# Kernel tuning notes

Hardware: AMD Instinct MI355X
Metric: run time of the kernel (lower is better)

The kernel has to match this reference:

```python
import jax, jax.numpy as jnp
import numpy as np

D_MODEL = 1472
N_HEADS = 6
D_KV = 64
INNER = N_HEADS * D_KV
NUM_BUCKETS = 32
MAX_DIST = 128


def _relative_position_bucket(relative_position, bidirectional=True,
                              num_buckets=NUM_BUCKETS, max_distance=MAX_DIST):
    ret = jnp.zeros_like(relative_position)
    if bidirectional:
        num_buckets //= 2
        ret = ret + (relative_position > 0).astype(jnp.int32) * num_buckets
        rel = jnp.abs(relative_position)
    else:
        rel = -jnp.minimum(relative_position, 0)
    max_exact = num_buckets // 2
    is_small = rel < max_exact
    rel_f = jnp.maximum(rel, 1).astype(jnp.float32)
    large = max_exact + (
        jnp.log(rel_f / max_exact) / np.log(max_distance / max_exact)
        * (num_buckets - max_exact)
    ).astype(jnp.int32)
    large = jnp.minimum(large, num_buckets - 1)
    return ret + jnp.where(is_small, rel, large)


def _position_bias(q_len, k_len, rel_bias):
    # rel_bias: [num_buckets, n_heads]
    ctx = jnp.arange(q_len)[:, None]
    mem = jnp.arange(k_len)[None, :]
    buckets = _relative_position_bucket(mem - ctx, bidirectional=True)
    values = rel_bias[buckets]                 # [Q, K, H]
    return jnp.transpose(values, (2, 0, 1))[None]  # [1, H, Q, K]


def setup_inputs() -> dict:
    key = jax.random.key(0)
    ks = jax.random.split(key, 8)
    B, S = 4, 2048
    scale = 0.02
    return {
        "kv_sequences": jax.random.normal(ks[0], (B, S, D_MODEL), jnp.float32),
        "q_sequences": jax.random.normal(ks[1], (B, S, D_MODEL), jnp.float32),
        "mask": jnp.zeros((B, 1, S, S), jnp.float32),
        "WQ": jax.random.normal(ks[2], (D_MODEL, INNER), jnp.float32) * scale,
        "WK": jax.random.normal(ks[3], (D_MODEL, INNER), jnp.float32) * scale,
        "WV": jax.random.normal(ks[4], (D_MODEL, INNER), jnp.float32) * scale,
        "WO": jax.random.normal(ks[5], (INNER, D_MODEL), jnp.float32) * scale,
        "rel_bias": jax.random.normal(ks[6], (NUM_BUCKETS, N_HEADS), jnp.float32) * scale,
    }


def reference(kv_sequences, q_sequences, mask, WQ, WK, WV, WO, rel_bias):
    B, Kl, _ = kv_sequences.shape
    Ql = q_sequences.shape[1]
    # projections -> [B, H, L, d_kv]
    q = (q_sequences @ WQ).reshape(B, Ql, N_HEADS, D_KV).transpose(0, 2, 1, 3)
    k = (kv_sequences @ WK).reshape(B, Kl, N_HEADS, D_KV).transpose(0, 2, 1, 3)
    v = (kv_sequences @ WV).reshape(B, Kl, N_HEADS, D_KV).transpose(0, 2, 1, 3)
    # T5-style: no 1/sqrt(d) scaling
    logits = jnp.einsum("bhqd,bhkd->bhqk", q, k)
    logits = logits + _position_bias(Ql, Kl, rel_bias)
    logits = logits + mask
    attn = jax.nn.softmax(logits.astype(jnp.float32), axis=-1).astype(logits.dtype)
    out = jnp.einsum("bhqk,bhkd->bhqd", attn, v)
    out = out.transpose(0, 2, 1, 3).reshape(B, Ql, INNER)
    return out @ WO
```

## Files before the change

kernel.cpp:

```cpp
#include <hip/hip_runtime.h>
#include <hip/hip_fp16.h>
#include <cstdint>

#define DM    1472
#define NH    6
#define DKV   64
#define INNER 384
#define BATCH 4
#define SEQ   2048
#define LOG2E 1.4426950408889634f

typedef __attribute__((ext_vector_type(8))) _Float16 half8;
typedef __attribute__((ext_vector_type(4))) _Float16 half4;
typedef __attribute__((ext_vector_type(4))) float f32x4;

__device__ __forceinline__ int swz64(int row, int b)  { return b ^ (((row >> 1) & 3) << 4); }
__device__ __forceinline__ int swz128(int row, int b) { return b ^ ((row & 7) << 4); }

__device__ __forceinline__ void gload16(const void* g, const void* l) {
  __builtin_amdgcn_global_load_lds((const __attribute__((address_space(1))) void*)g,
                                   (__attribute__((address_space(3))) void*)l, 16, 0, 0);
}

__global__ void prep_weights(const float* __restrict__ WQ, const float* __restrict__ WK,
                             const float* __restrict__ WV, const float* __restrict__ WO,
                             _Float16* __restrict__ WqT, _Float16* __restrict__ WkT,
                             _Float16* __restrict__ WvT, _Float16* __restrict__ WoT) {
  int idx = blockIdx.x * blockDim.x + threadIdx.x;
  const int per = DM * INNER;
  if (idx >= 4 * per) return;
  int which = idx / per;
  int i = idx - which * per;
  if (which < 3) {
    const float* W = which == 0 ? WQ : (which == 1 ? WK : WV);
    _Float16* T = which == 0 ? WqT : (which == 1 ? WkT : WvT);
    int k = i / INNER, n = i - (i / INNER) * INNER;
    T[(size_t)n * DM + k] = (_Float16)W[i];
  } else {
    int k = i / DM, n = i - (i / DM) * DM;
    WoT[(size_t)n * INNER + k] = (_Float16)WO[i];
  }
}

__global__ void prep_bias(const float* __restrict__ rel_bias, float* __restrict__ biasS) {
  int idx = blockIdx.x * blockDim.x + threadIdx.x;
  const int TOT = NH * 4 * 4104;
  if (idx >= TOT) return;
  int h = idx / (4 * 4104);
  int rem = idx - h * 4 * 4104;
  int cc = rem / 4104;
  int i = rem - cc * 4104;
  int j = i + cc; if (j > 4094) j = 4094;
  int d = j - 2047;
  int ret = d > 0 ? 16 : 0;
  int a = d < 0 ? -d : d;
  int bucket;
  if (a < 8) bucket = ret + a;
  else {
    int large;
    if      (a >= 91) large = 15;
    else if (a >= 64) large = 14;
    else if (a >= 46) large = 13;
    else if (a >= 32) large = 12;
    else if (a >= 23) large = 11;
    else if (a >= 16) large = 10;
    else if (a >= 12) large = 9;
    else              large = 8;
    bucket = ret + large;
  }
  biasS[idx] = rel_bias[bucket * NH + h] * LOG2E;
}

__global__ __launch_bounds__(256) void proj_gemm(
    const float* __restrict__ Xq, const float* __restrict__ Xkv,
    const _Float16* __restrict__ WqT, const _Float16* __restrict__ WkvT,
    _Float16* __restrict__ Qo, _Float16* __restrict__ Ko, _Float16* __restrict__ Vto) {
  const int bm = blockIdx.x, by = blockIdx.y;
  const bool isQ = by < 3;
  const float* __restrict__ X = isQ ? Xq : Xkv;
  const _Float16* __restrict__ WT = isQ ? (WqT + (size_t)by * 128 * DM)
                                        : (WkvT + (size_t)(by - 3) * 128 * DM);

  __shared__ alignas(16) float    As[2][128 * 32];
  __shared__ alignas(16) _Float16 Bs[2][128 * 32];

  const int tid = threadIdx.x;
  const int lane = tid & 63, wave = tid >> 6;
  const int wm = wave >> 1, wn = wave & 1;
  const int l15 = lane & 15, lg = lane >> 4;

  f32x4 acc[4][4] = {};

  const int aoff = 4 * ((lane & 7) ^ (lane >> 3));
  const float* asrc[4];
#pragma unroll
  for (int c = 0; c < 4; ++c)
    asrc[c] = X + (size_t)(bm * 128 + (wave * 4 + c) * 8 + (lane >> 3)) * DM + aoff;
  const int boff = 8 * ((lane & 3) ^ ((lane >> 3) & 3));
  const _Float16* bsrc[2];
#pragma unroll
  for (int c = 0; c < 2; ++c)
    bsrc[c] = WT + (size_t)((wave * 2 + c) * 16 + (lane >> 2)) * DM + boff;

  const int NT = DM / 32;

#pragma unroll
  for (int c = 0; c < 4; ++c)
    gload16(asrc[c], (const char*)&As[0][0] + (wave * 4 + c) * 1024);
#pragma unroll
  for (int c = 0; c < 2; ++c)
    gload16(bsrc[c], (const char*)&Bs[0][0] + (wave * 2 + c) * 1024);
  __syncthreads();

  for (int t = 0; t < NT; ++t) {
    if (t + 1 < NT) {
      const int nb = (t + 1) & 1;
      const int kf = (t + 1) * 32;
#pragma unroll
      for (int c = 0; c < 4; ++c)
        gload16(asrc[c] + kf, (const char*)&As[nb][0] + (wave * 4 + c) * 1024);
#pragma unroll
      for (int c = 0; c < 2; ++c)
        gload16(bsrc[c] + kf, (const char*)&Bs[nb][0] + (wave * 2 + c) * 1024);
    }

    const char* Ab = (const char*)&As[t & 1][0];
    const char* Bb = (const char*)&Bs[t & 1][0];
    half8 af[4], bf[4];
#pragma unroll
    for (int m = 0; m < 4; ++m) {
      int r = wm * 64 + m * 16 + l15;
      int s = (r & 7) << 4;
      f32x4 x0 = *(const f32x4*)(Ab + r * 128 + ((lg * 32) ^ s));
      f32x4 x1 = *(const f32x4*)(Ab + r * 128 + ((lg * 32 + 16) ^ s));
      half8 h;
#pragma unroll
      for (int j = 0; j < 4; ++j) { h[j] = (_Float16)x0[j]; h[4 + j] = (_Float16)x1[j]; }
      af[m] = h;
    }
#pragma unroll
    for (int n = 0; n < 4; ++n) {
      int r = wn * 64 + n * 16 + l15;
      bf[n] = *(const half8*)(Bb + r * 64 + ((lg * 16) ^ (((r >> 1) & 3) << 4)));
    }

    __builtin_amdgcn_s_setprio(1);
#pragma unroll
    for (int m = 0; m < 4; ++m)
#pragma unroll
      for (int n = 0; n < 4; ++n)
        acc[m][n] = __builtin_amdgcn_mfma_f32_16x16x32_f16(af[m], bf[n], acc[m][n], 0, 0, 0);
    __builtin_amdgcn_s_setprio(0);

    __syncthreads();
  }

#pragma unroll
  for (int m = 0; m < 4; ++m)
#pragma unroll
    for (int n = 0; n < 4; ++n)
#pragma unroll
      for (int r = 0; r < 4; ++r) {
        int gm = bm * 128 + wm * 64 + m * 16 + lg * 4 + r;
        int gnl = wn * 64 + n * 16 + l15;
        int b = gm >> 11, s = gm & 2047;
        float av = acc[m][n][r];
        if (isQ) {
          int gn = by * 128 + gnl;
          int h = gn >> 6, dd = gn & 63;
          Qo[((size_t)(b * NH + h) * SEQ + s) * DKV + dd] = (_Float16)(av * LOG2E);
        } else {
          int gn = (by - 3) * 128 + gnl;
          if (gn < INNER) {
            int h = gn >> 6, dd = gn & 63;
            Ko[((size_t)(b * NH + h) * SEQ + s) * DKV + dd] = (_Float16)av;
          } else {
            int gnv = gn - INNER;
            int h = gnv >> 6, dd = gnv & 63;
            Vto[((size_t)(b * NH + h) * DKV + dd) * SEQ + s] = (_Float16)av;
          }
        }
      }
}

__global__ __launch_bounds__(256) void attn_kernel(
    const _Float16* __restrict__ Q, const _Float16* __restrict__ K, const _Float16* __restrict__ Vt,
    const float* __restrict__ biasS, const float* __restrict__ mask, _Float16* __restrict__ AO) {
  const int bid = blockIdx.x;
  const int g = (bid & 7) * 96 + (bid >> 3);
  const int bh = g >> 5, qb = g & 31;
  const int b = bh / NH, h = bh - b * NH;
  const int q0 = qb * 64;
  const int tid = threadIdx.x, lane = tid & 63, wave = tid >> 6;
  const int l15 = lane & 15, lg = lane >> 4;

  __shared__ alignas(16) _Float16 Ks[2][64 * 64];
  __shared__ alignas(16) _Float16 Vs[2][64 * 64];
  __shared__ alignas(16) _Float16 Ps[4][16 * 72];

  const size_t bhS = (size_t)bh * SEQ;
  const int qq = q0 + wave * 16 + l15;

  const _Float16* Qbase = Q + (bhS + q0 + wave * 16) * DKV;
  half8 qf0 = *(const half8*)(Qbase + (size_t)l15 * DKV + lg * 8);
  half8 qf1 = *(const half8*)(Qbase + (size_t)l15 * DKV + 32 + lg * 8);

  const float* maskrow = mask + (size_t)b * SEQ * SEQ + (size_t)qq * SEQ;
  const int c = (3 - l15) & 3;
  const float* bptr[4];
#pragma unroll
  for (int nf = 0; nf < 4; ++nf)
    bptr[nf] = biasS + (size_t)(h * 4 + c) * 4104 + (nf * 16 + lg * 4 - qq + 2047 - c);

  float m_r = -1e30f, l_r = 0.f;
  f32x4 oacc[4] = {};

  const int srow = tid >> 2;
  const int scb = (tid & 3) * 32;
  const _Float16* Ksrc = K + (bhS + srow) * DKV + (scb >> 1);
  const _Float16* Vsrc = Vt + ((size_t)bh * DKV + srow) * SEQ + (scb >> 1);

  {
    half8 k0v = *(const half8*)(Ksrc);
    half8 k1v = *(const half8*)(Ksrc + 8);
    half8 v0v = *(const half8*)(Vsrc);
    half8 v1v = *(const half8*)(Vsrc + 8);
    char* KsW = (char*)&Ks[0][0];
    char* VsW = (char*)&Vs[0][0];
    *(half8*)(KsW + srow * 128 + swz128(srow, scb)) = k0v;
    *(half8*)(KsW + srow * 128 + swz128(srow, scb + 16)) = k1v;
    *(half8*)(VsW + srow * 128 + swz128(srow, scb)) = v0v;
    *(half8*)(VsW + srow * 128 + swz128(srow, scb + 16)) = v1v;
  }

  for (int t = 0; t < SEQ / 64; ++t) {
    __syncthreads();
    const int kt = t * 64;
    const bool pre = (t + 1 < SEQ / 64);
    half8 knA, knB, vnA, vnB;
    if (pre) {
      const _Float16* kp = Ksrc + (size_t)(kt + 64) * DKV;
      knA = *(const half8*)(kp);
      knB = *(const half8*)(kp + 8);
      const _Float16* vp = Vsrc + kt + 64;
      vnA = *(const half8*)(vp);
      vnB = *(const half8*)(vp + 8);
    }
    const char* KsB = (const char*)&Ks[t & 1][0];
    const char* VsB = (const char*)&Vs[t & 1][0];
    char* PsB = (char*)&Ps[wave][0];

    f32x4 sacc[4] = {};
    __builtin_amdgcn_s_setprio(1);
#pragma unroll
    for (int nf = 0; nf < 4; ++nf) {
      int kr = nf * 16 + l15;
      half8 kf0 = *(const half8*)(KsB + kr * 128 + swz128(kr, lg * 16));
      half8 kf1 = *(const half8*)(KsB + kr * 128 + swz128(kr, 64 + lg * 16));
      sacc[nf] = __builtin_amdgcn_mfma_f32_16x16x32_f16(kf0, qf0, sacc[nf], 0, 0, 0);
      sacc[nf] = __builtin_amdgcn_mfma_f32_16x16x32_f16(kf1, qf1, sacc[nf], 0, 0, 0);
    }
    __builtin_amdgcn_s_setprio(0);

    float sv[4][4];
    float mx = -1e30f;
#pragma unroll
    for (int nf = 0; nf < 4; ++nf) {
      f32x4 bv = *(const f32x4*)(bptr[nf] + kt);
      f32x4 mv = *(const f32x4*)(maskrow + kt + nf * 16 + lg * 4);
#pragma unroll
      for (int r = 0; r < 4; ++r) {
        float s = sacc[nf][r] + bv[r] + mv[r] * LOG2E;
        sv[nf][r] = s;
        mx = fmaxf(mx, s);
      }
    }
    mx = fmaxf(mx, __shfl_xor(mx, 16));
    mx = fmaxf(mx, __shfl_xor(mx, 32));
    const float mnew = fmaxf(m_r, mx);
    const float sc_ = __builtin_amdgcn_exp2f(m_r - mnew);
    float rs = 0.f;
#pragma unroll
    for (int nf = 0; nf < 4; ++nf) {
      half4 ph;
#pragma unroll
      for (int r = 0; r < 4; ++r) {
        float p = __builtin_amdgcn_exp2f(sv[nf][r] - mnew);
        rs += p;
        ph[r] = (_Float16)p;
      }
      *(half4*)(PsB + l15 * 144 + nf * 32 + lg * 8) = ph;
    }
    rs += __shfl_xor(rs, 16);
    rs += __shfl_xor(rs, 32);
    l_r = l_r * sc_ + rs;
    m_r = mnew;

    f32x4 scv;
#pragma unroll
    for (int r = 0; r < 4; ++r) scv[r] = __shfl(sc_, lg * 4 + r);
#pragma unroll
    for (int df = 0; df < 4; ++df) oacc[df] *= scv;

    __builtin_amdgcn_s_setprio(1);
#pragma unroll
    for (int ks = 0; ks < 2; ++ks) {
      half8 pa = *(const half8*)(PsB + l15 * 144 + ks * 64 + lg * 16);
#pragma unroll
      for (int df = 0; df < 4; ++df) {
        int vr = df * 16 + l15;
        half8 vb = *(const half8*)(VsB + vr * 128 + swz128(vr, ks * 64 + lg * 16));
        oacc[df] = __builtin_amdgcn_mfma_f32_16x16x32_f16(pa, vb, oacc[df], 0, 0, 0);
      }
    }
    __builtin_amdgcn_s_setprio(0);

    if (pre) {
      char* KsW = (char*)&Ks[(t + 1) & 1][0];
      char* VsW = (char*)&Vs[(t + 1) & 1][0];
      *(half8*)(KsW + srow * 128 + swz128(srow, scb)) = knA;
      *(half8*)(KsW + srow * 128 + swz128(srow, scb + 16)) = knB;
      *(half8*)(VsW + srow * 128 + swz128(srow, scb)) = vnA;
      *(half8*)(VsW + srow * 128 + swz128(srow, scb + 16)) = vnB;
    }
  }

  f32x4 lv;
#pragma unroll
  for (int r = 0; r < 4; ++r) lv[r] = __shfl(l_r, lg * 4 + r);
#pragma unroll
  for (int df = 0; df < 4; ++df) {
    int dd = df * 16 + l15;
#pragma unroll
    for (int r = 0; r < 4; ++r) {
      int qrow = q0 + wave * 16 + lg * 4 + r;
      AO[((size_t)(b * SEQ + qrow)) * INNER + h * DKV + dd] = (_Float16)(oacc[df][r] / lv[r]);
    }
  }
}

__global__ __launch_bounds__(256) void out_gemm(
    const _Float16* __restrict__ A, const _Float16* __restrict__ BT, float* __restrict__ C) {
  __shared__ alignas(16) _Float16 As[2][128 * 32];
  __shared__ alignas(16) _Float16 Bs[2][64 * 32];

  const int tid = threadIdx.x, lane = tid & 63, wave = tid >> 6;
  const int wm = wave >> 1, wn = wave & 1;
  const int bm = blockIdx.x, bn = blockIdx.y;
  const int l15 = lane & 15, lg = lane >> 4;

  f32x4 acc[4][2] = {};
  const int arow = tid >> 1, aseg = tid & 1;
  const int brow = tid >> 2, bchunk = tid & 3;
  const _Float16* asrc = A + (size_t)(bm * 128 + arow) * INNER + aseg * 16;
  const _Float16* bsrc = BT + (size_t)(bn * 64 + brow) * INNER + bchunk * 8;

  const int NT = INNER / 32;

  {
    half8 a0 = *(const half8*)(asrc);
    half8 a1 = *(const half8*)(asrc + 8);
    half8 b0 = *(const half8*)(bsrc);
    char* AsW = (char*)&As[0][0];
    char* BsW = (char*)&Bs[0][0];
    *(half8*)(AsW + arow * 64 + swz64(arow, aseg * 32)) = a0;
    *(half8*)(AsW + arow * 64 + swz64(arow, aseg * 32 + 16)) = a1;
    *(half8*)(BsW + brow * 64 + swz64(brow, bchunk * 16)) = b0;
  }

  for (int t = 0; t < NT; ++t) {
    __syncthreads();
    const bool pre = (t + 1 < NT);
    half8 na0, na1, nb0;
    if (pre) {
      const int kn = (t + 1) * 32;
      na0 = *(const half8*)(asrc + kn);
      na1 = *(const half8*)(asrc + kn + 8);
      nb0 = *(const half8*)(bsrc + kn);
    }

    const char* AsB = (const char*)&As[t & 1][0];
    const char* BsB = (const char*)&Bs[t & 1][0];
    half8 af[4], bf[2];
#pragma unroll
    for (int m = 0; m < 4; ++m) {
      int r = wm * 64 + m * 16 + l15;
      af[m] = *(const half8*)(AsB + r * 64 + swz64(r, lg * 16));
    }
#pragma unroll
    for (int n = 0; n < 2; ++n) {
      int r = wn * 32 + n * 16 + l15;
      bf[n] = *(const half8*)(BsB + r * 64 + swz64(r, lg * 16));
    }
    __builtin_amdgcn_s_setprio(1);
#pragma unroll
    for (int m = 0; m < 4; ++m)
#pragma unroll
      for (int n = 0; n < 2; ++n)
        acc[m][n] = __builtin_amdgcn_mfma_f32_16x16x32_f16(af[m], bf[n], acc[m][n], 0, 0, 0);
    __builtin_amdgcn_s_setprio(0);

    if (pre) {
      char* AsW = (char*)&As[(t + 1) & 1][0];
      char* BsW = (char*)&Bs[(t + 1) & 1][0];
      *(half8*)(AsW + arow * 64 + swz64(arow, aseg * 32)) = na0;
      *(half8*)(AsW + arow * 64 + swz64(arow, aseg * 32 + 16)) = na1;
      *(half8*)(BsW + brow * 64 + swz64(brow, bchunk * 16)) = nb0;
    }
  }

#pragma unroll
  for (int m = 0; m < 4; ++m)
#pragma unroll
    for (int n = 0; n < 2; ++n)
#pragma unroll
      for (int r = 0; r < 4; ++r) {
        int gm = bm * 128 + wm * 64 + m * 16 + lg * 4 + r;
        int gn = bn * 64 + wn * 32 + n * 16 + l15;
        C[(size_t)gm * DM + gn] = acc[m][n][r];
      }
}

extern "C" void kernel_launch(void* const* d_in, const int* in_sizes, int n_in,
                              void* d_out, int out_size, void* d_ws, size_t ws_size,
                              hipStream_t stream) {
  const float* kv   = (const float*)d_in[0];
  const float* qs   = (const float*)d_in[1];
  const float* mask = (const float*)d_in[2];
  const float* WQ   = (const float*)d_in[3];
  const float* WK   = (const float*)d_in[4];
  const float* WV   = (const float*)d_in[5];
  const float* WO   = (const float*)d_in[6];
  const float* rb   = (const float*)d_in[7];
  float* out = (float*)d_out;
  char* ws = (char*)d_ws;

  const size_t WT_BYTES  = (size_t)INNER * DM * 2;
  const size_t QKV_BYTES = (size_t)BATCH * NH * SEQ * DKV * 2;
  _Float16* WqT = (_Float16*)(ws);
  _Float16* WkT = (_Float16*)(ws + WT_BYTES);
  _Float16* WvT = (_Float16*)(ws + 2 * WT_BYTES);
  _Float16* WoT = (_Float16*)(ws + 3 * WT_BYTES);
  _Float16* Qh  = (_Float16*)(ws + 4 * WT_BYTES);
  _Float16* Kh  = (_Float16*)(ws + 4 * WT_BYTES + QKV_BYTES);
  _Float16* Vth = (_Float16*)(ws + 4 * WT_BYTES + 2 * QKV_BYTES);
  _Float16* AO  = (_Float16*)(ws + 4 * WT_BYTES + 3 * QKV_BYTES);
  float* biasS  = (float*)(ws + 4 * WT_BYTES + 4 * QKV_BYTES);

  hipLaunchKernelGGL(prep_weights, dim3((4 * DM * INNER + 255) / 256), dim3(256), 0, stream,
                     WQ, WK, WV, WO, WqT, WkT, WvT, WoT);
  hipLaunchKernelGGL(prep_bias, dim3((NH * 4 * 4104 + 255) / 256), dim3(256), 0, stream, rb, biasS);
  hipLaunchKernelGGL(proj_gemm, dim3(64, 9), dim3(256), 0, stream,
                     qs, kv, WqT, WkT, Qh, Kh, Vth);
  hipLaunchKernelGGL(attn_kernel, dim3(768), dim3(256), 0, stream,
                     Qh, Kh, Vth, biasS, mask, AO);
  hipLaunchKernelGGL(out_gemm, dim3(64, 23), dim3(256), 0, stream, AO, WoT, out);
}
```

Baseline: 194.6 us.

## Widen attention KV tiles to 128 with lazy rescaling and single-buffered LDS

The attention kernel now processes 128 keys per iteration instead of 64, with a single LDS buffer for K and V, two barriers per iteration, and register prefetch of the next tile. Mask loads are issued before the QK MFMAs. The online-softmax rescale of the accumulator is skipped unless some row max grows by more than 8 (log2 units), and the P tile in LDS gets an XOR swizzle. Launch bounds request 3 blocks per CU. The aim is to halve loop and barrier overhead and cut rescale work, at the cost of more registers, an extra barrier per tile, and less overlap from dropping double buffering.

Measured after the change: 211.7 us. 8.8% more time.

```diff
diff --git a/kernel.cpp b/kernel.cpp
--- a/kernel.cpp
+++ b/kernel.cpp
@@ -183,7 +183,7 @@
       }
 }
 
-__global__ __launch_bounds__(256) void attn_kernel(
+__global__ __launch_bounds__(256, 3) void attn_kernel(
     const _Float16* __restrict__ Q, const _Float16* __restrict__ K, const _Float16* __restrict__ Vt,
     const float* __restrict__ biasS, const float* __restrict__ mask, _Float16* __restrict__ AO) {
   const int bid = blockIdx.x;
@@ -194,9 +194,9 @@
   const int tid = threadIdx.x, lane = tid & 63, wave = tid >> 6;
   const int l15 = lane & 15, lg = lane >> 4;
 
-  __shared__ alignas(16) _Float16 Ks[2][64 * 64];
-  __shared__ alignas(16) _Float16 Vs[2][64 * 64];
-  __shared__ alignas(16) _Float16 Ps[4][16 * 72];
+  __shared__ alignas(16) _Float16 Ks[128 * 64];
+  __shared__ alignas(16) _Float16 Vs[64 * 128];
+  __shared__ alignas(16) _Float16 Ps[4][16 * 128];
 
   const size_t bhS = (size_t)bh * SEQ;
   const int qq = q0 + wave * 16 + l15;
@@ -205,124 +205,132 @@
   half8 qf0 = *(const half8*)(Qbase + (size_t)l15 * DKV + lg * 8);
   half8 qf1 = *(const half8*)(Qbase + (size_t)l15 * DKV + 32 + lg * 8);
 
-  const float* maskrow = mask + (size_t)b * SEQ * SEQ + (size_t)qq * SEQ;
+  const float* maskrow = mask + (size_t)b * SEQ * SEQ + (size_t)qq * SEQ + lg * 4;
   const int c = (3 - l15) & 3;
-  const float* bptr[4];
-#pragma unroll
-  for (int nf = 0; nf < 4; ++nf)
-    bptr[nf] = biasS + (size_t)(h * 4 + c) * 4104 + (nf * 16 + lg * 4 - qq + 2047 - c);
+  const float* bbase = biasS + (size_t)(h * 4 + c) * 4104 + (lg * 4 - qq + 2047 - c);
 
   float m_r = -1e30f, l_r = 0.f;
   f32x4 oacc[4] = {};
 
-  const int srow = tid >> 2;
-  const int scb = (tid & 3) * 32;
-  const _Float16* Ksrc = K + (bhS + srow) * DKV + (scb >> 1);
-  const _Float16* Vsrc = Vt + ((size_t)bh * DKV + srow) * SEQ + (scb >> 1);
+  const int krow = tid >> 1, kc0 = (tid & 1) * 4;
+  const int vrow = tid >> 2, vc0 = (tid & 3) * 4;
+  const _Float16* Vg = Vt + ((size_t)bh * DKV + vrow) * SEQ;
+  char* KsB = (char*)Ks;
+  char* VsB = (char*)Vs;
+  char* PsB = (char*)&Ps[wave][0];
 
   {
-    half8 k0v = *(const half8*)(Ksrc);
-    half8 k1v = *(const half8*)(Ksrc + 8);
-    half8 v0v = *(const half8*)(Vsrc);
-    half8 v1v = *(const half8*)(Vsrc + 8);
-    char* KsW = (char*)&Ks[0][0];
-    char* VsW = (char*)&Vs[0][0];
-    *(half8*)(KsW + srow * 128 + swz128(srow, scb)) = k0v;
-    *(half8*)(KsW + srow * 128 + swz128(srow, scb + 16)) = k1v;
-    *(half8*)(VsW + srow * 128 + swz128(srow, scb)) = v0v;
-    *(half8*)(VsW + srow * 128 + swz128(srow, scb + 16)) = v1v;
-  }
-
-  for (int t = 0; t < SEQ / 64; ++t) {
-    __syncthreads();
-    const int kt = t * 64;
-    const bool pre = (t + 1 < SEQ / 64);
-    half8 knA, knB, vnA, vnB;
-    if (pre) {
-      const _Float16* kp = Ksrc + (size_t)(kt + 64) * DKV;
-      knA = *(const half8*)(kp);
-      knB = *(const half8*)(kp + 8);
-      const _Float16* vp = Vsrc + kt + 64;
-      vnA = *(const half8*)(vp);
-      vnB = *(const half8*)(vp + 8);
-    }
-    const char* KsB = (const char*)&Ks[t & 1][0];
-    const char* VsB = (const char*)&Vs[t & 1][0];
-    char* PsB = (char*)&Ps[wave][0];
-
-    f32x4 sacc[4] = {};
+    half8 kn[4], vn[4];
+#pragma unroll
+    for (int j = 0; j < 4; ++j) {
+      kn[j] = *(const half8*)(K + (bhS + krow) * DKV + (kc0 + j) * 8);
+      vn[j] = *(const half8*)(Vg + (vc0 + j) * 8);
+    }
+#pragma unroll
+    for (int j = 0; j < 4; ++j) {
+      *(half8*)(KsB + krow * 128 + (((kc0 + j) ^ (krow & 7)) << 4)) = kn[j];
+      *(half8*)(VsB + vrow * 256 + (((vc0 + j) ^ (vrow & 15)) << 4)) = vn[j];
+    }
+  }
+  __syncthreads();
+
+  const int NTI = SEQ / 128;
+  for (int t = 0; t < NTI; ++t) {
+    const int kt = t * 128;
+
+    half8 kn[4], vn[4];
+    if (t + 1 < NTI) {
+      const int knx = kt + 128;
+#pragma unroll
+      for (int j = 0; j < 4; ++j) {
+        kn[j] = *(const half8*)(K + (bhS + knx + krow) * DKV + (kc0 + j) * 8);
+        vn[j] = *(const half8*)(Vg + knx + (vc0 + j) * 8);
+      }
+    }
+    f32x4 mcur[8];
+#pragma unroll
+    for (int nf = 0; nf < 8; ++nf)
+      mcur[nf] = *(const f32x4*)(maskrow + kt + nf * 16);
+
+    f32x4 sacc[8] = {};
     __builtin_amdgcn_s_setprio(1);
 #pragma unroll
-    for (int nf = 0; nf < 4; ++nf) {
+    for (int nf = 0; nf < 8; ++nf) {
       int kr = nf * 16 + l15;
-      half8 kf0 = *(const half8*)(KsB + kr * 128 + swz128(kr, lg * 16));
-      half8 kf1 = *(const half8*)(KsB + kr * 128 + swz128(kr, 64 + lg * 16));
+      const char* rb = KsB + kr * 128;
+      int sw = kr & 7;
+      half8 kf0 = *(const half8*)(rb + ((lg ^ sw) << 4));
+      half8 kf1 = *(const half8*)(rb + (((4 + lg) ^ sw) << 4));
       sacc[nf] = __builtin_amdgcn_mfma_f32_16x16x32_f16(kf0, qf0, sacc[nf], 0, 0, 0);
       sacc[nf] = __builtin_amdgcn_mfma_f32_16x16x32_f16(kf1, qf1, sacc[nf], 0, 0, 0);
     }
     __builtin_amdgcn_s_setprio(0);
 
-    float sv[4][4];
-    float mx = -1e30f;
-#pragma unroll
-    for (int nf = 0; nf < 4; ++nf) {
-      f32x4 bv = *(const f32x4*)(bptr[nf] + kt);
-      f32x4 mv = *(const f32x4*)(maskrow + kt + nf * 16 + lg * 4);
-#pragma unroll
-      for (int r = 0; r < 4; ++r) {
-        float s = sacc[nf][r] + bv[r] + mv[r] * LOG2E;
-        sv[nf][r] = s;
-        mx = fmaxf(mx, s);
-      }
-    }
+    float sv[8][4];
+    float fm[8];
+#pragma unroll
+    for (int nf = 0; nf < 8; ++nf) {
+      f32x4 bv = *(const f32x4*)(bbase + kt + nf * 16);
+#pragma unroll
+      for (int r = 0; r < 4; ++r)
+        sv[nf][r] = sacc[nf][r] + bv[r] + mcur[nf][r] * LOG2E;
+      fm[nf] = fmaxf(fmaxf(sv[nf][0], sv[nf][1]), fmaxf(sv[nf][2], sv[nf][3]));
+    }
+    float mx = fmaxf(fmaxf(fmaxf(fm[0], fm[1]), fmaxf(fm[2], fm[3])),
+                     fmaxf(fmaxf(fm[4], fm[5]), fmaxf(fm[6], fm[7])));
     mx = fmaxf(mx, __shfl_xor(mx, 16));
     mx = fmaxf(mx, __shfl_xor(mx, 32));
-    const float mnew = fmaxf(m_r, mx);
-    const float sc_ = __builtin_amdgcn_exp2f(m_r - mnew);
+
+    if (!__all(mx <= m_r + 8.0f)) {
+      float mnew = fmaxf(m_r, mx);
+      float sc_ = __builtin_amdgcn_exp2f(m_r - mnew);
+      m_r = mnew;
+      l_r *= sc_;
+      f32x4 scv;
+#pragma unroll
+      for (int r = 0; r < 4; ++r) scv[r] = __shfl(sc_, lg * 4 + r);
+#pragma unroll
+      for (int df = 0; df < 4; ++df) oacc[df] *= scv;
+    }
+
     float rs = 0.f;
 #pragma unroll
-    for (int nf = 0; nf < 4; ++nf) {
+    for (int nf = 0; nf < 8; ++nf) {
       half4 ph;
 #pragma unroll
       for (int r = 0; r < 4; ++r) {
-        float p = __builtin_amdgcn_exp2f(sv[nf][r] - mnew);
+        float p = __builtin_amdgcn_exp2f(sv[nf][r] - m_r);
         rs += p;
         ph[r] = (_Float16)p;
       }
-      *(half4*)(PsB + l15 * 144 + nf * 32 + lg * 8) = ph;
+      *(half4*)(PsB + l15 * 256 + ((((nf * 2 + (lg >> 1)) ^ l15) << 4) + (lg & 1) * 8)) = ph;
     }
     rs += __shfl_xor(rs, 16);
     rs += __shfl_xor(rs, 32);
-    l_r = l_r * sc_ + rs;
-    m_r = mnew;
-
-    f32x4 scv;
-#pragma unroll
-    for (int r = 0; r < 4; ++r) scv[r] = __shfl(sc_, lg * 4 + r);
-#pragma unroll
-    for (int df = 0; df < 4; ++df) oacc[df] *= scv;
+    l_r += rs;
 
     __builtin_amdgcn_s_setprio(1);
 #pragma unroll
-    for (int ks = 0; ks < 2; ++ks) {
-      half8 pa = *(const half8*)(PsB + l15 * 144 + ks * 64 + lg * 16);
+    for (int ks = 0; ks < 4; ++ks) {
+      half8 pa = *(const half8*)(PsB + l15 * 256 + (((ks * 4 + lg) ^ l15) << 4));
 #pragma unroll
       for (int df = 0; df < 4; ++df) {
         int vr = df * 16 + l15;
-        half8 vb = *(const half8*)(VsB + vr * 128 + swz128(vr, ks * 64 + lg * 16));
+        half8 vb = *(const half8*)(VsB + vr * 256 + (((ks * 4 + lg) ^ (vr & 15)) << 4));
         oacc[df] = __builtin_amdgcn_mfma_f32_16x16x32_f16(pa, vb, oacc[df], 0, 0, 0);
       }
     }
     __builtin_amdgcn_s_setprio(0);
 
-    if (pre) {
-      char* KsW = (char*)&Ks[(t + 1) & 1][0];
-      char* VsW = (char*)&Vs[(t + 1) & 1][0];
-      *(half8*)(KsW + srow * 128 + swz128(srow, scb)) = knA;
-      *(half8*)(KsW + srow * 128 + swz128(srow, scb + 16)) = knB;
-      *(half8*)(VsW + srow * 128 + swz128(srow, scb)) = vnA;
-      *(half8*)(VsW + srow * 128 + swz128(srow, scb + 16)) = vnB;
-    }
+    __syncthreads();
+    if (t + 1 < NTI) {
+#pragma unroll
+      for (int j = 0; j < 4; ++j) {
+        *(half8*)(KsB + krow * 128 + (((kc0 + j) ^ (krow & 7)) << 4)) = kn[j];
+        *(half8*)(VsB + vrow * 256 + (((vc0 + j) ^ (vrow & 15)) << 4)) = vn[j];
+      }
+    }
+    __syncthreads();
   }
 
   f32x4 lv;
```

## Prefetch mask/bias one tile ahead, lazy softmax rescale, defer row-sum reduction

Applied to the files above, without the earlier changes.

Mask and relative-bias tiles are now loaded one iteration ahead into registers, so their global latency overlaps the QK MFMAs instead of stalling the softmax. The online softmax only rescales the accumulator and running max when some row's max grows by more than 8 (log2 units), skipping the shuffles and multiplies on most tiles. Per-lane row sums are accumulated locally and reduced across lanes once at the end. It also sets a 3-waves occupancy launch bound and unrolls the loop by 2, which raises register pressure and could cause spills.

After: 194.6 us. About the same (-0.0%).

```diff
diff --git a/kernel.cpp b/kernel.cpp
--- a/kernel.cpp
+++ b/kernel.cpp
@@ -183,7 +183,7 @@
       }
 }
 
-__global__ __launch_bounds__(256) void attn_kernel(
+__global__ __launch_bounds__(256, 3) void attn_kernel(
     const _Float16* __restrict__ Q, const _Float16* __restrict__ K, const _Float16* __restrict__ Vt,
     const float* __restrict__ biasS, const float* __restrict__ mask, _Float16* __restrict__ AO) {
   const int bid = blockIdx.x;
@@ -205,14 +205,11 @@
   half8 qf0 = *(const half8*)(Qbase + (size_t)l15 * DKV + lg * 8);
   half8 qf1 = *(const half8*)(Qbase + (size_t)l15 * DKV + 32 + lg * 8);
 
-  const float* maskrow = mask + (size_t)b * SEQ * SEQ + (size_t)qq * SEQ;
+  const float* maskrow = mask + (size_t)b * SEQ * SEQ + (size_t)qq * SEQ + lg * 4;
   const int c = (3 - l15) & 3;
-  const float* bptr[4];
-#pragma unroll
-  for (int nf = 0; nf < 4; ++nf)
-    bptr[nf] = biasS + (size_t)(h * 4 + c) * 4104 + (nf * 16 + lg * 4 - qq + 2047 - c);
-
-  float m_r = -1e30f, l_r = 0.f;
+  const float* bbase = biasS + (size_t)(h * 4 + c) * 4104 + (lg * 4 - qq + 2047 - c);
+
+  float m_r = -1e30f, l_acc = 0.f;
   f32x4 oacc[4] = {};
 
   const int srow = tid >> 2;
@@ -233,11 +230,20 @@
     *(half8*)(VsW + srow * 128 + swz128(srow, scb + 16)) = v1v;
   }
 
+  f32x4 mc[4], bc[4];
+#pragma unroll
+  for (int nf = 0; nf < 4; ++nf) {
+    mc[nf] = *(const f32x4*)(maskrow + nf * 16);
+    bc[nf] = *(const f32x4*)(bbase + nf * 16);
+  }
+
+#pragma unroll 2
   for (int t = 0; t < SEQ / 64; ++t) {
     __syncthreads();
     const int kt = t * 64;
     const bool pre = (t + 1 < SEQ / 64);
     half8 knA, knB, vnA, vnB;
+    f32x4 mn[4], bn[4];
     if (pre) {
       const _Float16* kp = Ksrc + (size_t)(kt + 64) * DKV;
       knA = *(const half8*)(kp);
@@ -245,6 +251,11 @@
       const _Float16* vp = Vsrc + kt + 64;
       vnA = *(const half8*)(vp);
       vnB = *(const half8*)(vp + 8);
+#pragma unroll
+      for (int nf = 0; nf < 4; ++nf) {
+        mn[nf] = *(const f32x4*)(maskrow + kt + 64 + nf * 16);
+        bn[nf] = *(const f32x4*)(bbase + kt + 64 + nf * 16);
+      }
     }
     const char* KsB = (const char*)&Ks[t & 1][0];
     const char* VsB = (const char*)&Vs[t & 1][0];
@@ -263,44 +274,43 @@
     __builtin_amdgcn_s_setprio(0);
 
     float sv[4][4];
-    float mx = -1e30f;
+    float fm[4];
 #pragma unroll
     for (int nf = 0; nf < 4; ++nf) {
-      f32x4 bv = *(const f32x4*)(bptr[nf] + kt);
-      f32x4 mv = *(const f32x4*)(maskrow + kt + nf * 16 + lg * 4);
-#pragma unroll
-      for (int r = 0; r < 4; ++r) {
-        float s = sacc[nf][r] + bv[r] + mv[r] * LOG2E;
-        sv[nf][r] = s;
-        mx = fmaxf(mx, s);
-      }
-    }
+#pragma unroll
+      for (int r = 0; r < 4; ++r)
+        sv[nf][r] = sacc[nf][r] + bc[nf][r] + mc[nf][r] * LOG2E;
+      fm[nf] = fmaxf(fmaxf(sv[nf][0], sv[nf][1]), fmaxf(sv[nf][2], sv[nf][3]));
+    }
+    float mx = fmaxf(fmaxf(fm[0], fm[1]), fmaxf(fm[2], fm[3]));
     mx = fmaxf(mx, __shfl_xor(mx, 16));
     mx = fmaxf(mx, __shfl_xor(mx, 32));
-    const float mnew = fmaxf(m_r, mx);
-    const float sc_ = __builtin_amdgcn_exp2f(m_r - mnew);
+
+    if (!__all(mx <= m_r + 8.0f)) {
+      float mnew = fmaxf(m_r, mx);
+      float sc_ = __builtin_amdgcn_exp2f(m_r - mnew);
+      m_r = mnew;
+      l_acc *= sc_;
+      f32x4 scv;
+#pragma unroll
+      for (int r = 0; r < 4; ++r) scv[r] = __shfl(sc_, lg * 4 + r);
+#pragma unroll
+      for (int df = 0; df < 4; ++df) oacc[df] *= scv;
+    }
+
     float rs = 0.f;
 #pragma unroll
     for (int nf = 0; nf < 4; ++nf) {
       half4 ph;
 #pragma unroll
       for (int r = 0; r < 4; ++r) {
-        float p = __builtin_amdgcn_exp2f(sv[nf][r] - mnew);
+        float p = __builtin_amdgcn_exp2f(sv[nf][r] - m_r);
         rs += p;
         ph[r] = (_Float16)p;
       }
       *(half4*)(PsB + l15 * 144 + nf * 32 + lg * 8) = ph;
     }
-    rs += __shfl_xor(rs, 16);
-    rs += __shfl_xor(rs, 32);
-    l_r = l_r * sc_ + rs;
-    m_r = mnew;
-
-    f32x4 scv;
-#pragma unroll
-    for (int r = 0; r < 4; ++r) scv[r] = __shfl(sc_, lg * 4 + r);
-#pragma unroll
-    for (int df = 0; df < 4; ++df) oacc[df] *= scv;
+    l_acc += rs;
 
     __builtin_amdgcn_s_setprio(1);
 #pragma unroll
@@ -322,12 +332,16 @@
       *(half8*)(KsW + srow * 128 + swz128(srow, scb + 16)) = knB;
       *(half8*)(VsW + srow * 128 + swz128(srow, scb)) = vnA;
       *(half8*)(VsW + srow * 128 + swz128(srow, scb + 16)) = vnB;
-    }
-  }
-
+#pragma unroll
+      for (int nf = 0; nf < 4; ++nf) { mc[nf] = mn[nf]; bc[nf] = bn[nf]; }
+    }
+  }
+
+  l_acc += __shfl_xor(l_acc, 16);
+  l_acc += __shfl_xor(l_acc, 32);
   f32x4 lv;
 #pragma unroll
-  for (int r = 0; r < 4; ++r) lv[r] = __shfl(l_r, lg * 4 + r);
+  for (int r = 0; r < 4; ++r) lv[r] = __shfl(l_acc, lg * 4 + r);
 #pragma unroll
   for (int df = 0; df < 4; ++df) {
     int dd = df * 16 + l15;
```
